# Kernel optimization log

Measured on AMD Instinct MI355X. Metric: run time of the kernel, lower is better.

## Reference

```python
import jax, jax.numpy as jnp
import numpy as np

EPS = 1e-7  # same clamp torch BCE effectively applies to avoid log(0)


def _level_bce(att, boxes, valid, area, level_id, H, W):
    # att: [B, h_l, w_l] predicted attention in (0,1); boxes: [B, N, 4]; valid/area: [B, N]
    B, hl, wl = att.shape
    base = 2.0 ** (level_id + 5)
    min_area = base * base * 0.5
    max_area = (base * 1.58) ** 2 * 2.0
    sel = valid & (area >= min_area) & (area <= max_area)  # [B, N]
    sx = wl / W
    sy = hl / H
    # rasterization bounds on the level grid (int() == floor for non-negative coords)
    x1 = jnp.maximum(jnp.floor(boxes[..., 0] * sx), 0.0)
    y1 = jnp.maximum(jnp.floor(boxes[..., 1] * sy), 0.0)
    x2 = jnp.minimum(jnp.ceil(boxes[..., 2] * sx) + 1.0, float(wl))
    y2 = jnp.minimum(jnp.ceil(boxes[..., 3] * sy) + 1.0, float(hl))
    rows = jnp.arange(hl, dtype=att.dtype)
    cols = jnp.arange(wl, dtype=att.dtype)
    # separable per-box row/col indicators -> matmul-style OR to avoid a [B,N,h,w] tensor
    rin = (sel[..., None] & (rows >= y1[..., None]) & (rows < y2[..., None])).astype(att.dtype)  # [B,N,h]
    cin = (sel[..., None] & (cols >= x1[..., None]) & (cols < x2[..., None])).astype(att.dtype)  # [B,N,w]
    mask_gt = (jnp.einsum('bnh,bnw->bhw', rin, cin) > 0).astype(att.dtype)  # [B,h,w]
    p = jnp.clip(att, EPS, 1.0 - EPS)
    bce = -(mask_gt * jnp.log(p) + (1.0 - mask_gt) * jnp.log1p(-p))
    return bce.mean(axis=(1, 2))  # [B]


def reference(att0, att1, att2, att3, att4, bboxs, h, w):
    atts = [att0, att1, att2, att3, att4]
    hf = float(h)
    wf = float(w)
    x1, y1, x2, y2, label = (bboxs[..., i] for i in range(5))
    valid = (label != -1) & (x1 <= wf) & (y1 <= hf) & (x2 <= wf) & (y2 <= hf)  # [B,N]
    area = (x2 - x1) * (y2 - y1)
    boxes = bboxs[..., :4]
    per_level = [
        _level_bce(a[:, 0, :, :], boxes, valid, area, i, hf, wf)
        for i, a in enumerate(atts)
    ]
    sample_loss = jnp.stack(per_level, axis=0).mean(axis=0)  # [B]
    has_box = valid.any(axis=1)
    sample_loss = jnp.where(has_box, sample_loss, jnp.zeros_like(sample_loss))
    return sample_loss.mean(keepdims=True)  # [1]


def setup_inputs() -> dict:
    key = jax.random.key(0)
    ks = jax.random.split(key, 10)
    B, N, H, W = 16, 96, 4096, 4096
    sizes = [(1024, 1024), (512, 512), (256, 256), (128, 128), (64, 64)]
    inp = {}
    for i, (hl, wl) in enumerate(sizes):
        inp[f'att{i}'] = jax.random.uniform(ks[i], (B, 1, hl, wl), jnp.float32, 1e-4, 1.0 - 1e-4)
    cx = jax.random.uniform(ks[5], (B, N), jnp.float32) * W
    cy = jax.random.uniform(ks[6], (B, N), jnp.float32) * H
    side = jnp.exp(jax.random.uniform(ks[7], (B, N), jnp.float32, np.log(24.0), np.log(1100.0)))
    x1 = jnp.clip(cx - side / 2, 0.0, float(W))
    x2 = jnp.clip(cx + side / 2, 0.0, float(W))
    y1 = jnp.clip(cy - side / 2, 0.0, float(H))
    y2 = jnp.clip(cy + side / 2, 0.0, float(H))
    label = jnp.where(jax.random.uniform(ks[8], (B, N), jnp.float32) < 0.1, -1.0, 1.0)
    inp['bboxs'] = jnp.stack([x1, y1, x2, y2, label], axis=-1)
    inp['h'] = H
    inp['w'] = W
    return inp
```

## Files before the change

kernel.cpp:

```cpp
#include <hip/hip_runtime.h>

#define B_SZ 16
#define N_BOX 96
#define EPSF 1e-7f

#define MASK_BYTES 2793472u
#define ACC_STRIDE 32
#define ACC_BYTES  (B_SZ * 5 * ACC_STRIDE * 4)
#define CLEAR_F4   ((MASK_BYTES + ACC_BYTES) / 16u)

__device__ __forceinline__ unsigned level_bit_off(int l) {
    switch (l) {
        case 0:  return 0u;
        case 1:  return 16777216u;
        case 2:  return 20971520u;
        case 3:  return 22020096u;
        default: return 22282240u;
    }
}

__global__ __launch_bounds__(256)
void clear_kernel(uint4* __restrict__ ws)
{
    unsigned i = blockIdx.x * 256u + threadIdx.x;
    if (i < CLEAR_F4) ws[i] = make_uint4(0u, 0u, 0u, 0u);
}

__global__ __launch_bounds__(64)
void raster_kernel(const float* __restrict__ bboxs,
                   const int* __restrict__ hp, const int* __restrict__ wp,
                   unsigned* __restrict__ maskbits)
{
    int gid = blockIdx.x;
    int n = gid % N_BOX;
    int l = (gid / N_BOX) % 5;
    int b = gid / (N_BOX * 5);

    const float* bx = bboxs + (b * N_BOX + n) * 5;
    float x1 = bx[0], y1 = bx[1], x2 = bx[2], y2 = bx[3], lb = bx[4];
    float Wf = (float)(*wp), Hf = (float)(*hp);

    bool valid = (lb != -1.0f) && (x1 <= Wf) && (y1 <= Hf) && (x2 <= Wf) && (y2 <= Hf);
    if (!valid) return;

    float area = (x2 - x1) * (y2 - y1);
    double based = (double)(32 << l);
    float mn  = (float)(based * based * 0.5);
    float mxv = (float)((based * 1.58) * (based * 1.58) * 2.0);
    if (!(area >= mn && area <= mxv)) return;

    int wl = 1024 >> l;
    float sx = (float)wl / Wf;
    float sy = (float)wl / Hf;

    int ix1 = (int)fmaxf(floorf(x1 * sx), 0.0f);
    int iy1 = (int)fmaxf(floorf(y1 * sy), 0.0f);
    int ix2 = (int)fminf(ceilf(x2 * sx) + 1.0f, (float)wl);
    int iy2 = (int)fminf(ceilf(y2 * sy) + 1.0f, (float)wl);
    if (ix2 <= ix1 || iy2 <= iy1) return;

    unsigned bitOff = level_bit_off(l) + (unsigned)b * (unsigned)(wl * wl);
    int nrows = iy2 - iy1;
    for (int rr = (int)threadIdx.x; rr < nrows; rr += 64) {
        int r = iy1 + rr;
        unsigned rs = bitOff + (unsigned)r * (unsigned)wl + (unsigned)ix1;
        unsigned re = rs + (unsigned)(ix2 - ix1);
        unsigned w0 = rs >> 5, w1 = (re - 1u) >> 5;
        for (unsigned w = w0; w <= w1; ++w) {
            unsigned lo = (w == w0) ? (rs & 31u) : 0u;
            unsigned hi = (w == w1) ? (((re - 1u) & 31u) + 1u) : 32u;
            unsigned m = (hi == 32u ? 0xffffffffu : ((1u << hi) - 1u)) & ~((1u << lo) - 1u);
            atomicOr(&maskbits[w], m);
        }
    }
}

__global__ __launch_bounds__(256)
void bce_kernel(const float* __restrict__ a0, const float* __restrict__ a1,
                const float* __restrict__ a2, const float* __restrict__ a3,
                const float* __restrict__ a4,
                const unsigned* __restrict__ maskbits,
                float* __restrict__ acc)
{
    int bid = blockIdx.x;
    int l, start, bppShift;
    const float* att;
    if (bid < 2048)      { l = 0; start = 0;    bppShift = 7; att = a0; }
    else if (bid < 2560) { l = 1; start = 2048; bppShift = 5; att = a1; }
    else if (bid < 2688) { l = 2; start = 2560; bppShift = 3; att = a2; }
    else if (bid < 2720) { l = 3; start = 2688; bppShift = 1; att = a3; }
    else                 { l = 4; start = 2720; bppShift = 0; att = a4; }

    int planeF4 = 1 << (18 - 2 * l);
    int bil = bid - start;
    int b     = bil >> bppShift;
    int chunk = bil & ((1 << bppShift) - 1);
    int nf4   = planeF4 >> bppShift;
    unsigned gf4base = (unsigned)b * (unsigned)planeF4
                     + (unsigned)chunk * (unsigned)nf4 + threadIdx.x;
    unsigned lvlBit  = level_bit_off(l);

    float s = 0.0f;
    if (nf4 == 2048) {
        float4 av[8];
        unsigned nib[8];
        #pragma unroll
        for (int u = 0; u < 8; ++u) {
            unsigned gf4 = gf4base + (unsigned)(u * 256);
            av[u] = reinterpret_cast<const float4*>(att)[gf4];
            unsigned bidx = lvlBit + gf4 * 4u;
            nib[u] = (maskbits[bidx >> 5] >> (bidx & 31u)) & 0xFu;
        }
        #pragma unroll
        for (int u = 0; u < 8; ++u) {
            float pv[4] = {av[u].x, av[u].y, av[u].z, av[u].w};
            #pragma unroll
            for (int j = 0; j < 4; ++j) {
                float p = fminf(fmaxf(pv[j], EPSF), 1.0f - EPSF);
                float q = ((nib[u] >> j) & 1u) ? p : (1.0f - p);
                s -= __logf(q);
            }
        }
    } else {
        float4 av[4];
        unsigned nib[4];
        #pragma unroll
        for (int u = 0; u < 4; ++u) {
            unsigned gf4 = gf4base + (unsigned)(u * 256);
            av[u] = reinterpret_cast<const float4*>(att)[gf4];
            unsigned bidx = lvlBit + gf4 * 4u;
            nib[u] = (maskbits[bidx >> 5] >> (bidx & 31u)) & 0xFu;
        }
        #pragma unroll
        for (int u = 0; u < 4; ++u) {
            float pv[4] = {av[u].x, av[u].y, av[u].z, av[u].w};
            #pragma unroll
            for (int j = 0; j < 4; ++j) {
                float p = fminf(fmaxf(pv[j], EPSF), 1.0f - EPSF);
                float q = ((nib[u] >> j) & 1u) ? p : (1.0f - p);
                s -= __logf(q);
            }
        }
    }

    #pragma unroll
    for (int off = 32; off > 0; off >>= 1)
        s += __shfl_down(s, off, 64);
    __shared__ float wsum[4];
    int lane = threadIdx.x & 63, wv = threadIdx.x >> 6;
    if (lane == 0) wsum[wv] = s;
    __syncthreads();
    if (threadIdx.x == 0) {
        float t = wsum[0] + wsum[1] + wsum[2] + wsum[3];
        atomicAdd(&acc[(b * 5 + l) * ACC_STRIDE], t);
    }
}

__global__ __launch_bounds__(256)
void finalize_kernel(const float* __restrict__ bboxs,
                     const int* __restrict__ hp, const int* __restrict__ wp,
                     const float* __restrict__ acc, float* __restrict__ out)
{
    __shared__ int hasbox[B_SZ];
    if (threadIdx.x < B_SZ) hasbox[threadIdx.x] = 0;
    __syncthreads();
    float Wf = (float)(*wp), Hf = (float)(*hp);
    for (int i = (int)threadIdx.x; i < B_SZ * N_BOX; i += 256) {
        const float* bx = bboxs + i * 5;
        if (bx[4] != -1.0f && bx[0] <= Wf && bx[1] <= Hf && bx[2] <= Wf && bx[3] <= Hf)
            hasbox[i / N_BOX] = 1;
    }
    __syncthreads();
    if (threadIdx.x == 0) {
        double tot = 0.0;
        for (int b = 0; b < B_SZ; ++b) {
            if (!hasbox[b]) continue;
            double s = 0.0;
            for (int l = 0; l < 5; ++l) {
                int wl = 1024 >> l;
                s += (double)acc[(b * 5 + l) * ACC_STRIDE] / (double)(wl * wl);
            }
            tot += s / 5.0;
        }
        out[0] = (float)(tot / (double)B_SZ);
    }
}

extern "C" void kernel_launch(void* const* d_in, const int* in_sizes, int n_in,
                              void* d_out, int out_size, void* d_ws, size_t ws_size,
                              hipStream_t stream)
{
    const float* a0 = (const float*)d_in[0];
    const float* a1 = (const float*)d_in[1];
    const float* a2 = (const float*)d_in[2];
    const float* a3 = (const float*)d_in[3];
    const float* a4 = (const float*)d_in[4];
    const float* bboxs = (const float*)d_in[5];
    const int* hp = (const int*)d_in[6];
    const int* wp = (const int*)d_in[7];

    unsigned* maskbits = (unsigned*)d_ws;
    float* acc = (float*)((char*)d_ws + MASK_BYTES);

    clear_kernel<<<(CLEAR_F4 + 255u) / 256u, 256, 0, stream>>>((uint4*)d_ws);
    raster_kernel<<<B_SZ * 5 * N_BOX, 64, 0, stream>>>(bboxs, hp, wp, maskbits);
    bce_kernel<<<2736, 256, 0, stream>>>(a0, a1, a2, a3, a4, maskbits, acc);
    finalize_kernel<<<1, 256, 0, stream>>>(bboxs, hp, wp, acc, (float*)d_out);
}
```

Before: 41.47 us.

## Replace mask rasterization with background BCE plus per-box correction

Removes the mask clear and atomic rasterization kernels. The streaming pass now computes -log(1-p) for every pixel, and extra blocks (one per sample and level) add log(1-p)-log(p) for pixels inside selected boxes, skipping overlaps with earlier boxes. Per-block partial sums are written without atomics and reduced in double precision in finalize. This trades two launches and the mask traffic for serial box setup and an O(R^2) overlap check in the correction blocks, which could become the tail at the coarse levels.

```diff
diff --git a/kernel.cpp b/kernel.cpp
--- a/kernel.cpp
+++ b/kernel.cpp
@@ -4,141 +4,124 @@
 #define N_BOX 96
 #define EPSF 1e-7f
 
-#define MASK_BYTES 2793472u
-#define ACC_STRIDE 32
-#define ACC_BYTES  (B_SZ * 5 * ACC_STRIDE * 4)
-#define CLEAR_F4   ((MASK_BYTES + ACC_BYTES) / 16u)
-
-__device__ __forceinline__ unsigned level_bit_off(int l) {
-    switch (l) {
-        case 0:  return 0u;
-        case 1:  return 16777216u;
-        case 2:  return 20971520u;
-        case 3:  return 22020096u;
-        default: return 22282240u;
-    }
+#define N_STREAM 2736
+#define N_CORR   (B_SZ * 5)
+#define N_BLOCKS (N_STREAM + N_CORR)
+
+__device__ __forceinline__ const float* pick_att(
+    int l, const float* a0, const float* a1, const float* a2,
+    const float* a3, const float* a4)
+{
+    switch (l) { case 0: return a0; case 1: return a1; case 2: return a2;
+                 case 3: return a3; default: return a4; }
 }
 
 __global__ __launch_bounds__(256)
-void clear_kernel(uint4* __restrict__ ws)
-{
-    unsigned i = blockIdx.x * 256u + threadIdx.x;
-    if (i < CLEAR_F4) ws[i] = make_uint4(0u, 0u, 0u, 0u);
-}
-
-__global__ __launch_bounds__(64)
-void raster_kernel(const float* __restrict__ bboxs,
-                   const int* __restrict__ hp, const int* __restrict__ wp,
-                   unsigned* __restrict__ maskbits)
-{
-    int gid = blockIdx.x;
-    int n = gid % N_BOX;
-    int l = (gid / N_BOX) % 5;
-    int b = gid / (N_BOX * 5);
-
-    const float* bx = bboxs + (b * N_BOX + n) * 5;
-    float x1 = bx[0], y1 = bx[1], x2 = bx[2], y2 = bx[3], lb = bx[4];
-    float Wf = (float)(*wp), Hf = (float)(*hp);
-
-    bool valid = (lb != -1.0f) && (x1 <= Wf) && (y1 <= Hf) && (x2 <= Wf) && (y2 <= Hf);
-    if (!valid) return;
-
-    float area = (x2 - x1) * (y2 - y1);
-    double based = (double)(32 << l);
-    float mn  = (float)(based * based * 0.5);
-    float mxv = (float)((based * 1.58) * (based * 1.58) * 2.0);
-    if (!(area >= mn && area <= mxv)) return;
-
-    int wl = 1024 >> l;
-    float sx = (float)wl / Wf;
-    float sy = (float)wl / Hf;
-
-    int ix1 = (int)fmaxf(floorf(x1 * sx), 0.0f);
-    int iy1 = (int)fmaxf(floorf(y1 * sy), 0.0f);
-    int ix2 = (int)fminf(ceilf(x2 * sx) + 1.0f, (float)wl);
-    int iy2 = (int)fminf(ceilf(y2 * sy) + 1.0f, (float)wl);
-    if (ix2 <= ix1 || iy2 <= iy1) return;
-
-    unsigned bitOff = level_bit_off(l) + (unsigned)b * (unsigned)(wl * wl);
-    int nrows = iy2 - iy1;
-    for (int rr = (int)threadIdx.x; rr < nrows; rr += 64) {
-        int r = iy1 + rr;
-        unsigned rs = bitOff + (unsigned)r * (unsigned)wl + (unsigned)ix1;
-        unsigned re = rs + (unsigned)(ix2 - ix1);
-        unsigned w0 = rs >> 5, w1 = (re - 1u) >> 5;
-        for (unsigned w = w0; w <= w1; ++w) {
-            unsigned lo = (w == w0) ? (rs & 31u) : 0u;
-            unsigned hi = (w == w1) ? (((re - 1u) & 31u) + 1u) : 32u;
-            unsigned m = (hi == 32u ? 0xffffffffu : ((1u << hi) - 1u)) & ~((1u << lo) - 1u);
-            atomicOr(&maskbits[w], m);
-        }
-    }
-}
-
-__global__ __launch_bounds__(256)
-void bce_kernel(const float* __restrict__ a0, const float* __restrict__ a1,
-                const float* __restrict__ a2, const float* __restrict__ a3,
-                const float* __restrict__ a4,
-                const unsigned* __restrict__ maskbits,
-                float* __restrict__ acc)
-{
+void bce_all_kernel(const float* __restrict__ a0, const float* __restrict__ a1,
+                    const float* __restrict__ a2, const float* __restrict__ a3,
+                    const float* __restrict__ a4,
+                    const float* __restrict__ bboxs,
+                    const int* __restrict__ hp, const int* __restrict__ wp,
+                    float* __restrict__ partial,
+                    float* __restrict__ corr)
+{
+    __shared__ float wsum[4];
+    __shared__ int rx1[N_BOX], ry1[N_BOX], rx2[N_BOX], ry2[N_BOX];
+    __shared__ int Rcnt;
+
     int bid = blockIdx.x;
-    int l, start, bppShift;
-    const float* att;
-    if (bid < 2048)      { l = 0; start = 0;    bppShift = 7; att = a0; }
-    else if (bid < 2560) { l = 1; start = 2048; bppShift = 5; att = a1; }
-    else if (bid < 2688) { l = 2; start = 2560; bppShift = 3; att = a2; }
-    else if (bid < 2720) { l = 3; start = 2688; bppShift = 1; att = a3; }
-    else                 { l = 4; start = 2720; bppShift = 0; att = a4; }
-
-    int planeF4 = 1 << (18 - 2 * l);
-    int bil = bid - start;
-    int b     = bil >> bppShift;
-    int chunk = bil & ((1 << bppShift) - 1);
-    int nf4   = planeF4 >> bppShift;
-    unsigned gf4base = (unsigned)b * (unsigned)planeF4
-                     + (unsigned)chunk * (unsigned)nf4 + threadIdx.x;
-    unsigned lvlBit  = level_bit_off(l);
-
     float s = 0.0f;
-    if (nf4 == 2048) {
-        float4 av[8];
-        unsigned nib[8];
-        #pragma unroll
-        for (int u = 0; u < 8; ++u) {
-            unsigned gf4 = gf4base + (unsigned)(u * 256);
-            av[u] = reinterpret_cast<const float4*>(att)[gf4];
-            unsigned bidx = lvlBit + gf4 * 4u;
-            nib[u] = (maskbits[bidx >> 5] >> (bidx & 31u)) & 0xFu;
-        }
-        #pragma unroll
-        for (int u = 0; u < 8; ++u) {
-            float pv[4] = {av[u].x, av[u].y, av[u].z, av[u].w};
-            #pragma unroll
-            for (int j = 0; j < 4; ++j) {
-                float p = fminf(fmaxf(pv[j], EPSF), 1.0f - EPSF);
-                float q = ((nib[u] >> j) & 1u) ? p : (1.0f - p);
-                s -= __logf(q);
+
+    if (bid < N_STREAM) {
+        int l, start, bppShift;
+        const float* att;
+        if (bid < 2048)      { l = 0; start = 0;    bppShift = 7; att = a0; }
+        else if (bid < 2560) { l = 1; start = 2048; bppShift = 5; att = a1; }
+        else if (bid < 2688) { l = 2; start = 2560; bppShift = 3; att = a2; }
+        else if (bid < 2720) { l = 3; start = 2688; bppShift = 1; att = a3; }
+        else                 { l = 4; start = 2720; bppShift = 0; att = a4; }
+
+        int planeF4 = 1 << (18 - 2 * l);
+        int bil = bid - start;
+        int chunk = bil & ((1 << bppShift) - 1);
+        int nf4 = planeF4 >> bppShift;
+        unsigned gf4base = (unsigned)(bil >> bppShift) * (unsigned)planeF4
+                         + (unsigned)chunk * (unsigned)nf4 + threadIdx.x;
+
+        if (nf4 == 2048) {
+            float4 av[8];
+            #pragma unroll
+            for (int u = 0; u < 8; ++u)
+                av[u] = reinterpret_cast<const float4*>(att)[gf4base + u * 256u];
+            #pragma unroll
+            for (int u = 0; u < 8; ++u) {
+                float pv[4] = {av[u].x, av[u].y, av[u].z, av[u].w};
+                #pragma unroll
+                for (int j = 0; j < 4; ++j) {
+                    float p = fminf(fmaxf(pv[j], EPSF), 1.0f - EPSF);
+                    s -= __logf(1.0f - p);
+                }
+            }
+        } else {
+            float4 av[4];
+            #pragma unroll
+            for (int u = 0; u < 4; ++u)
+                av[u] = reinterpret_cast<const float4*>(att)[gf4base + u * 256u];
+            #pragma unroll
+            for (int u = 0; u < 4; ++u) {
+                float pv[4] = {av[u].x, av[u].y, av[u].z, av[u].w};
+                #pragma unroll
+                for (int j = 0; j < 4; ++j) {
+                    float p = fminf(fmaxf(pv[j], EPSF), 1.0f - EPSF);
+                    s -= __logf(1.0f - p);
+                }
             }
         }
     } else {
-        float4 av[4];
-        unsigned nib[4];
-        #pragma unroll
-        for (int u = 0; u < 4; ++u) {
-            unsigned gf4 = gf4base + (unsigned)(u * 256);
-            av[u] = reinterpret_cast<const float4*>(att)[gf4];
-            unsigned bidx = lvlBit + gf4 * 4u;
-            nib[u] = (maskbits[bidx >> 5] >> (bidx & 31u)) & 0xFu;
-        }
-        #pragma unroll
-        for (int u = 0; u < 4; ++u) {
-            float pv[4] = {av[u].x, av[u].y, av[u].z, av[u].w};
-            #pragma unroll
-            for (int j = 0; j < 4; ++j) {
-                float p = fminf(fmaxf(pv[j], EPSF), 1.0f - EPSF);
-                float q = ((nib[u] >> j) & 1u) ? p : (1.0f - p);
-                s -= __logf(q);
+        int idx = bid - N_STREAM;
+        int b = idx / 5, l = idx % 5;
+        const float* att = pick_att(l, a0, a1, a2, a3, a4);
+        int wl = 1024 >> l;
+        float Wf = (float)(*wp), Hf = (float)(*hp);
+
+        if (threadIdx.x == 0) {
+            int R = 0;
+            double based = (double)(32 << l);
+            float mn  = (float)(based * based * 0.5);
+            float mxv = (float)((based * 1.58) * (based * 1.58) * 2.0);
+            float sx = (float)wl / Wf, sy = (float)wl / Hf;
+            for (int n = 0; n < N_BOX; ++n) {
+                const float* bx = bboxs + (b * N_BOX + n) * 5;
+                float x1 = bx[0], y1 = bx[1], x2 = bx[2], y2 = bx[3], lb = bx[4];
+                if (!(lb != -1.0f && x1 <= Wf && y1 <= Hf && x2 <= Wf && y2 <= Hf))
+                    continue;
+                float area = (x2 - x1) * (y2 - y1);
+                if (!(area >= mn && area <= mxv)) continue;
+                int ix1 = (int)fmaxf(floorf(x1 * sx), 0.0f);
+                int iy1 = (int)fmaxf(floorf(y1 * sy), 0.0f);
+                int ix2 = (int)fminf(ceilf(x2 * sx) + 1.0f, (float)wl);
+                int iy2 = (int)fminf(ceilf(y2 * sy) + 1.0f, (float)wl);
+                if (ix2 <= ix1 || iy2 <= iy1) continue;
+                rx1[R] = ix1; ry1[R] = iy1; rx2[R] = ix2; ry2[R] = iy2; ++R;
+            }
+            Rcnt = R;
+        }
+        __syncthreads();
+
+        unsigned pbase = (unsigned)b << (20 - 2 * l);
+        for (int r = 0; r < Rcnt; ++r) {
+            int w = rx2[r] - rx1[r];
+            int npx = w * (ry2[r] - ry1[r]);
+            for (int i = (int)threadIdx.x; i < npx; i += 256) {
+                int y = ry1[r] + i / w;
+                int x = rx1[r] + i % w;
+                bool dup = false;
+                for (int q = 0; q < r; ++q)
+                    dup |= (x >= rx1[q] && x < rx2[q] && y >= ry1[q] && y < ry2[q]);
+                if (dup) continue;
+                float p = att[pbase + (unsigned)y * (unsigned)wl + (unsigned)x];
+                p = fminf(fmaxf(p, EPSF), 1.0f - EPSF);
+                s += __logf(1.0f - p) - __logf(p);
             }
         }
     }
@@ -146,22 +129,25 @@
     #pragma unroll
     for (int off = 32; off > 0; off >>= 1)
         s += __shfl_down(s, off, 64);
-    __shared__ float wsum[4];
     int lane = threadIdx.x & 63, wv = threadIdx.x >> 6;
     if (lane == 0) wsum[wv] = s;
     __syncthreads();
     if (threadIdx.x == 0) {
         float t = wsum[0] + wsum[1] + wsum[2] + wsum[3];
-        atomicAdd(&acc[(b * 5 + l) * ACC_STRIDE], t);
+        if (bid < N_STREAM) partial[bid] = t;
+        else                corr[bid - N_STREAM] = t;
     }
 }
 
 __global__ __launch_bounds__(256)
 void finalize_kernel(const float* __restrict__ bboxs,
                      const int* __restrict__ hp, const int* __restrict__ wp,
-                     const float* __restrict__ acc, float* __restrict__ out)
+                     const float* __restrict__ partial,
+                     const float* __restrict__ corr,
+                     float* __restrict__ out)
 {
     __shared__ int hasbox[B_SZ];
+    __shared__ double red[256];
     if (threadIdx.x < B_SZ) hasbox[threadIdx.x] = 0;
     __syncthreads();
     float Wf = (float)(*wp), Hf = (float)(*hp);
@@ -171,19 +157,36 @@
             hasbox[i / N_BOX] = 1;
     }
     __syncthreads();
-    if (threadIdx.x == 0) {
-        double tot = 0.0;
-        for (int b = 0; b < B_SZ; ++b) {
-            if (!hasbox[b]) continue;
-            double s = 0.0;
-            for (int l = 0; l < 5; ++l) {
-                int wl = 1024 >> l;
-                s += (double)acc[(b * 5 + l) * ACC_STRIDE] / (double)(wl * wl);
-            }
-            tot += s / 5.0;
-        }
-        out[0] = (float)(tot / (double)B_SZ);
-    }
+
+    double t = 0.0;
+    for (int i = (int)threadIdx.x; i < N_STREAM; i += 256) {
+        int l, start, bppShift;
+        if (i < 2048)      { l = 0; start = 0;    bppShift = 7; }
+        else if (i < 2560) { l = 1; start = 2048; bppShift = 5; }
+        else if (i < 2688) { l = 2; start = 2560; bppShift = 3; }
+        else if (i < 2720) { l = 3; start = 2688; bppShift = 1; }
+        else               { l = 4; start = 2720; bppShift = 0; }
+        int b = (i - start) >> bppShift;
+        if (hasbox[b]) {
+            int wl = 1024 >> l;
+            t += (double)partial[i] / (double)(wl * wl);
+        }
+    }
+    for (int i = (int)threadIdx.x; i < N_CORR; i += 256) {
+        int b = i / 5, l = i % 5;
+        if (hasbox[b]) {
+            int wl = 1024 >> l;
+            t += (double)corr[i] / (double)(wl * wl);
+        }
+    }
+    red[threadIdx.x] = t;
+    __syncthreads();
+    for (int off = 128; off > 0; off >>= 1) {
+        if ((int)threadIdx.x < off) red[threadIdx.x] += red[threadIdx.x + off];
+        __syncthreads();
+    }
+    if (threadIdx.x == 0)
+        out[0] = (float)(red[0] / (5.0 * (double)B_SZ));
 }
 
 extern "C" void kernel_launch(void* const* d_in, const int* in_sizes, int n_in,
@@ -199,11 +202,11 @@
     const int* hp = (const int*)d_in[6];
     const int* wp = (const int*)d_in[7];
 
-    unsigned* maskbits = (unsigned*)d_ws;
-    float* acc = (float*)((char*)d_ws + MASK_BYTES);
-
-    clear_kernel<<<(CLEAR_F4 + 255u) / 256u, 256, 0, stream>>>((uint4*)d_ws);
-    raster_kernel<<<B_SZ * 5 * N_BOX, 64, 0, stream>>>(bboxs, hp, wp, maskbits);
-    bce_kernel<<<2736, 256, 0, stream>>>(a0, a1, a2, a3, a4, maskbits, acc);
-    finalize_kernel<<<1, 256, 0, stream>>>(bboxs, hp, wp, acc, (float*)d_out);
-}
+    float* partial = (float*)d_ws;
+    float* corr    = partial + N_STREAM;
+
+    bce_all_kernel<<<N_BLOCKS, 256, 0, stream>>>(a0, a1, a2, a3, a4,
+                                                 bboxs, hp, wp, partial, corr);
+    finalize_kernel<<<1, 256, 0, stream>>>(bboxs, hp, wp, partial, corr,
+                                           (float*)d_out);
+}
```

Result: slower. 158.3 us (+281.6%).
